# Kernel tuning notes

Measured on AMD Instinct MI355X. Metric: run time of the kernel, lower is better.

Reference implementation:

```python
import jax, jax.numpy as jnp
import numpy as np

B, T = 4, 2048          # batch, seq_len
D, H = 2048, 4096       # input_dim, router hidden_dim
E, O = 16, 2048         # num_experts, expert_output_dim
TAU = 0.5               # forward default tau


def setup_inputs() -> dict:
    key = jax.random.key(0)
    kx, k1, k2, k3, k4, k5, k6 = jax.random.split(key, 7)
    s = 0.02
    return {
        "x": jax.random.normal(kx, (B, T, D), dtype=jnp.float32),
        "W1": jax.random.normal(k1, (D, H), dtype=jnp.float32) * s,
        "b1": jnp.zeros((H,), dtype=jnp.float32),
        "W2": jax.random.normal(k2, (H, E), dtype=jnp.float32) * s,
        "b2": jnp.zeros((E,), dtype=jnp.float32),
        "We": jax.random.normal(k3, (E, D, O), dtype=jnp.float32) * s,
        "be": jnp.zeros((E, O), dtype=jnp.float32),
    }


def reference(x, W1, b1, W2, b2, We, be):
    # Router: Linear -> ReLU -> Linear -> softmax
    h = jax.nn.relu(jnp.einsum("btd,dh->bth", x, W1) + b1)
    logits = jnp.einsum("bth,he->bte", h, W2) + b2
    probs = jax.nn.softmax(logits, axis=-1)                 # [B,T,E]
    max_p = jnp.max(probs, axis=-1, keepdims=True)
    mask = probs >= TAU * max_p                              # [B,T,E] bool
    k_per_token = jnp.sum(mask, axis=-1)                     # [B,T] int
    gates = jnp.where(mask, probs, 0.0)                      # masked router probs
    # Per-expert dense Linear, masked weighted accumulate (E=16 is a fixed,
    # structurally distinct set; loop is over experts, not data dims).
    out = jnp.zeros((B, T, O), dtype=x.dtype)
    for i in range(E):
        expert_out = jnp.einsum("btd,do->bto", x, We[i]) + be[i]
        out = out + gates[..., i:i + 1] * expert_out
    return out, k_per_token
```

## Files before the change

### kernel.cpp

```cpp
#include <hip/hip_runtime.h>
#include <stdint.h>

#define M_TOK 8192
#define DDIM  2048
#define HDIM  4096
#define NEXP  16
#define ODIM  2048

typedef __attribute__((ext_vector_type(8))) __bf16 bf16x8;
typedef __attribute__((ext_vector_type(4))) float  f32x4;

__device__ __forceinline__ unsigned short f2bf(float f) {
    unsigned int u = __float_as_uint(f);
    unsigned int r = (u + 0x7FFFu + ((u >> 16) & 1u)) >> 16;
    return (unsigned short)r;
}
__device__ __forceinline__ float bf2f(unsigned short s) {
    return __uint_as_float(((unsigned int)s) << 16);
}


__global__ void split_x_kernel(const float* __restrict__ x,
                               ushort* __restrict__ xh, ushort* __restrict__ xl) {
    size_t i = ((size_t)blockIdx.x * 256 + threadIdx.x) * 4;
    float4 v = *(const float4*)(x + i);
    float f[4] = {v.x, v.y, v.z, v.w};
    ushort hu[4], lu[4];
#pragma unroll
    for (int u = 0; u < 4; ++u) {
        hu[u] = f2bf(f[u]);
        lu[u] = f2bf(f[u] - bf2f(hu[u]));
    }
    *(ushort4*)(xh + i) = make_ushort4(hu[0], hu[1], hu[2], hu[3]);
    *(ushort4*)(xl + i) = make_ushort4(lu[0], lu[1], lu[2], lu[3]);
}

__global__ void transpose_split_w1_kernel(const float* __restrict__ W1,
                                          ushort* __restrict__ th, ushort* __restrict__ tl) {
    __shared__ float tile[64][65];
    int h0 = (blockIdx.x & 63) * 64;
    int d0 = (blockIdx.x >> 6) * 64;
    int r = threadIdx.x >> 4;
    int c = (threadIdx.x & 15) * 4;
#pragma unroll
    for (int rr = 0; rr < 4; ++rr) {
        int row = rr * 16 + r;
        float4 v = *(const float4*)(W1 + (size_t)(d0 + row) * HDIM + h0 + c);
        tile[row][c + 0] = v.x; tile[row][c + 1] = v.y;
        tile[row][c + 2] = v.z; tile[row][c + 3] = v.w;
    }
    __syncthreads();
#pragma unroll
    for (int rr = 0; rr < 4; ++rr) {
        int hrow = rr * 16 + r;
        ushort hu[4], lu[4];
#pragma unroll
        for (int u = 0; u < 4; ++u) {
            float f = tile[c + u][hrow];
            hu[u] = f2bf(f);
            lu[u] = f2bf(f - bf2f(hu[u]));
        }
        size_t o = (size_t)(h0 + hrow) * DDIM + d0 + c;
        *(ushort4*)(th + o) = make_ushort4(hu[0], hu[1], hu[2], hu[3]);
        *(ushort4*)(tl + o) = make_ushort4(lu[0], lu[1], lu[2], lu[3]);
    }
}

__global__ void transpose_we_kernel(const float* __restrict__ We, ushort* __restrict__ wt) {
    __shared__ float tile[64][65];
    int e = blockIdx.y;
    int o0 = (blockIdx.x & 31) * 64;
    int d0 = (blockIdx.x >> 5) * 64;
    const float* src = We + (size_t)e * DDIM * ODIM;
    ushort* dst = wt + (size_t)e * ODIM * DDIM;
    int r = threadIdx.x >> 4;
    int c = (threadIdx.x & 15) * 4;
#pragma unroll
    for (int rr = 0; rr < 4; ++rr) {
        int row = rr * 16 + r;
        float4 v = *(const float4*)(src + (size_t)(d0 + row) * ODIM + o0 + c);
        tile[row][c + 0] = v.x; tile[row][c + 1] = v.y;
        tile[row][c + 2] = v.z; tile[row][c + 3] = v.w;
    }
    __syncthreads();
#pragma unroll
    for (int rr = 0; rr < 4; ++rr) {
        int orow = rr * 16 + r;
        ushort hu[4];
#pragma unroll
        for (int u = 0; u < 4; ++u) hu[u] = f2bf(tile[c + u][orow]);
        *(ushort4*)(dst + (size_t)(o0 + orow) * DDIM + d0 + c) =
            make_ushort4(hu[0], hu[1], hu[2], hu[3]);
    }
}


__device__ __forceinline__ void stage_tile(const ushort* __restrict__ g0, int ld,
                                           ushort* lds0, int wave, int lane) {
#pragma unroll
    for (int j = 0; j < 4; ++j) {
        int L = wave * 256 + j * 64 + lane;
        int m = L >> 3;
        int kc = (L & 7) ^ (m & 7);
        const ushort* gp = g0 + (size_t)m * ld + kc * 8;
        ushort* lp = lds0 + (size_t)(wave * 256 + j * 64) * 8;
        __builtin_amdgcn_global_load_lds(
            (const __attribute__((address_space(1))) void*)gp,
            (__attribute__((address_space(3))) void*)lp, 16, 0, 0);
    }
}

__device__ __forceinline__ bf16x8 ldfrag(const ushort* lds0, int row, int kc) {
    return *(const bf16x8*)(lds0 + ((row << 3) + (kc ^ (row & 7))) * 8);
}

__global__ __launch_bounds__(256, 2) void gemm1_kernel(
    const ushort* __restrict__ xh, const ushort* __restrict__ xl,
    const ushort* __restrict__ wh, const ushort* __restrict__ wl,
    const float* __restrict__ b1, float* __restrict__ hout) {
    __shared__ ushort As[8192];
    __shared__ ushort Bs[8192];
    const int tile_m = (blockIdx.x & 63) << 7;
    const int tile_n = (blockIdx.x >> 6) << 7;
    const int tid = threadIdx.x;
    const int wave = tid >> 6, lane = tid & 63;
    const int q = lane >> 4, mrow = lane & 15;
    const int wm = (wave >> 1) << 6, wn = (wave & 1) << 6;
    f32x4 acc[4][4];
#pragma unroll
    for (int i = 0; i < 4; ++i)
#pragma unroll
        for (int j = 0; j < 4; ++j) acc[i][j] = {0.f, 0.f, 0.f, 0.f};

    for (int it = 0; it < 96; ++it) {
        const int phase = it >> 5;
        const ushort* Ab = (phase == 1) ? xl : xh;
        const ushort* Bb = (phase == 2) ? wl : wh;
        const int k0 = (it & 31) << 6;
        __syncthreads();
        stage_tile(Ab + (size_t)tile_m * DDIM + k0, DDIM, As, wave, lane);
        stage_tile(Bb + (size_t)tile_n * DDIM + k0, DDIM, Bs, wave, lane);
        __syncthreads();
#pragma unroll
        for (int s = 0; s < 2; ++s) {
            bf16x8 af[4], bfr[4];
#pragma unroll
            for (int i = 0; i < 4; ++i) af[i] = ldfrag(As, wm + i * 16 + mrow, s * 4 + q);
#pragma unroll
            for (int j = 0; j < 4; ++j) bfr[j] = ldfrag(Bs, wn + j * 16 + mrow, s * 4 + q);
#pragma unroll
            for (int i = 0; i < 4; ++i)
#pragma unroll
                for (int j = 0; j < 4; ++j)
                    acc[i][j] = __builtin_amdgcn_mfma_f32_16x16x32_bf16(
                        af[i], bfr[j], acc[i][j], 0, 0, 0);
        }
    }
#pragma unroll
    for (int i = 0; i < 4; ++i) {
        const int r0 = tile_m + wm + i * 16 + q * 4;
#pragma unroll
        for (int j = 0; j < 4; ++j) {
            const int cc = tile_n + wn + j * 16 + mrow;
            const float bb = b1[cc];
#pragma unroll
            for (int r = 0; r < 4; ++r) {
                float v = acc[i][j][r] + bb;
                hout[(size_t)(r0 + r) * HDIM + cc] = v > 0.f ? v : 0.f;
            }
        }
    }
}

__global__ void gemm2_kernel(const float* __restrict__ h, const float* __restrict__ W2,
                             const float* __restrict__ b2, float* __restrict__ logits) {
    const int e = threadIdx.x & 15;
    const int t = blockIdx.x * 16 + (threadIdx.x >> 4);
    const float* hr = h + (size_t)t * HDIM;
    float acc = 0.f;
    for (int d = 0; d < HDIM; d += 8) {
#pragma unroll
        for (int u = 0; u < 8; ++u)
            acc = fmaf(hr[d + u], W2[(size_t)(d + u) * NEXP + e], acc);
    }
    logits[(size_t)t * NEXP + e] = acc + b2[e];
}

__global__ void gates_kernel(const float* __restrict__ logits,
                             float* __restrict__ gates, float* __restrict__ kout,
                             int* __restrict__ cnt, int* __restrict__ list) {
    const int t = blockIdx.x * 256 + threadIdx.x;
    float l[16];
    const float4* lp = (const float4*)(logits + (size_t)t * 16);
#pragma unroll
    for (int i = 0; i < 4; ++i) {
        float4 v = lp[i];
        l[i * 4] = v.x; l[i * 4 + 1] = v.y; l[i * 4 + 2] = v.z; l[i * 4 + 3] = v.w;
    }
    float lmax = l[0];
#pragma unroll
    for (int i = 1; i < 16; ++i) lmax = fmaxf(lmax, l[i]);
    float p[16], S = 0.f;
#pragma unroll
    for (int i = 0; i < 16; ++i) { p[i] = expf(l[i] - lmax); S += p[i]; }
#pragma unroll
    for (int i = 0; i < 16; ++i) p[i] /= S;
    float pmax = p[0];
#pragma unroll
    for (int i = 1; i < 16; ++i) pmax = fmaxf(pmax, p[i]);
    const float thr = 0.5f * pmax;
    int k = 0;
    float g[16];
#pragma unroll
    for (int i = 0; i < 16; ++i) {
        bool m = p[i] >= thr;
        g[i] = m ? p[i] : 0.f;
        k += m ? 1 : 0;
        if (m) {
            int pos = atomicAdd(&cnt[i], 1);
            list[i * M_TOK + pos] = t;
        }
    }
    float4* gp = (float4*)(gates + (size_t)t * 16);
#pragma unroll
    for (int i = 0; i < 4; ++i)
        gp[i] = make_float4(g[i * 4], g[i * 4 + 1], g[i * 4 + 2], g[i * 4 + 3]);
    kout[t] = (float)k;
}

__global__ void init_out_kernel(const float* __restrict__ gates,
                                const float* __restrict__ be, float* __restrict__ out) {
    const int t = blockIdx.x;
    const int tid = threadIdx.x;
    __shared__ float g[16];
    if (tid < 16) g[tid] = gates[(size_t)t * 16 + tid];
    __syncthreads();
    const int c0 = tid * 8;
    float a[8] = {0.f, 0.f, 0.f, 0.f, 0.f, 0.f, 0.f, 0.f};
#pragma unroll
    for (int e = 0; e < 16; ++e) {
        float ge = g[e];
        if (ge != 0.f) {
            float4 v1 = *(const float4*)(be + (size_t)e * ODIM + c0);
            float4 v2 = *(const float4*)(be + (size_t)e * ODIM + c0 + 4);
            a[0] = fmaf(ge, v1.x, a[0]); a[1] = fmaf(ge, v1.y, a[1]);
            a[2] = fmaf(ge, v1.z, a[2]); a[3] = fmaf(ge, v1.w, a[3]);
            a[4] = fmaf(ge, v2.x, a[4]); a[5] = fmaf(ge, v2.y, a[5]);
            a[6] = fmaf(ge, v2.z, a[6]); a[7] = fmaf(ge, v2.w, a[7]);
        }
    }
    *(float4*)(out + (size_t)t * ODIM + c0)     = make_float4(a[0], a[1], a[2], a[3]);
    *(float4*)(out + (size_t)t * ODIM + c0 + 4) = make_float4(a[4], a[5], a[6], a[7]);
}

__global__ __launch_bounds__(256, 3) void moe_sparse_kernel(
    const ushort* __restrict__ xh, const ushort* __restrict__ weT,
    const float* __restrict__ gates, const int* __restrict__ cnt,
    const int* __restrict__ list, float* __restrict__ out) {
    const int bx = blockIdx.x;
    const int e = bx >> 10;
    const int chunk = (bx >> 4) & 63;
    const int ntile = bx & 15;
    const int ce = cnt[e];
    const int row0 = chunk << 7;
    if (row0 >= ce) return;
    const int rows = min(128, ce - row0);

    __shared__ ushort As[8192];
    __shared__ ushort Bs[8192];
    __shared__ int toks[128];
    __shared__ float gv[128];

    const int tid = threadIdx.x;
    if (tid < 128) {
        int t = list[e * M_TOK + row0 + min(tid, rows - 1)];
        toks[tid] = t;
        gv[tid] = gates[(size_t)t * NEXP + e];
    }
    __syncthreads();

    const int wave = tid >> 6, lane = tid & 63;
    const int q = lane >> 4, mrow = lane & 15;
    const int wm = (wave >> 1) << 6, wn = (wave & 1) << 6;

    const ushort* agp[4];
    const ushort* bgp[4];
    ushort* alp[4];
    ushort* blp[4];
    const ushort* wbase = weT + ((size_t)e * ODIM + (ntile << 7)) * DDIM;
#pragma unroll
    for (int j = 0; j < 4; ++j) {
        int L = wave * 256 + j * 64 + lane;
        int m = L >> 3;
        int kc = (L & 7) ^ (m & 7);
        agp[j] = xh + (size_t)toks[m] * DDIM + kc * 8;
        bgp[j] = wbase + (size_t)m * DDIM + kc * 8;
        alp[j] = As + (size_t)L * 8;
        blp[j] = Bs + (size_t)L * 8;
    }

    f32x4 acc[4][4];
#pragma unroll
    for (int i = 0; i < 4; ++i)
#pragma unroll
        for (int j = 0; j < 4; ++j) acc[i][j] = {0.f, 0.f, 0.f, 0.f};

    for (int it = 0; it < 32; ++it) {
        const int k0 = it << 6;
        __syncthreads();
#pragma unroll
        for (int j = 0; j < 4; ++j) {
            __builtin_amdgcn_global_load_lds(
                (const __attribute__((address_space(1))) void*)(agp[j] + k0),
                (__attribute__((address_space(3))) void*)alp[j], 16, 0, 0);
            __builtin_amdgcn_global_load_lds(
                (const __attribute__((address_space(1))) void*)(bgp[j] + k0),
                (__attribute__((address_space(3))) void*)blp[j], 16, 0, 0);
        }
        __syncthreads();
#pragma unroll
        for (int s = 0; s < 2; ++s) {
            bf16x8 af[4], bfr[4];
#pragma unroll
            for (int i = 0; i < 4; ++i) af[i] = ldfrag(As, wm + i * 16 + mrow, s * 4 + q);
#pragma unroll
            for (int j = 0; j < 4; ++j) bfr[j] = ldfrag(Bs, wn + j * 16 + mrow, s * 4 + q);
#pragma unroll
            for (int i = 0; i < 4; ++i)
#pragma unroll
                for (int j = 0; j < 4; ++j)
                    acc[i][j] = __builtin_amdgcn_mfma_f32_16x16x32_bf16(
                        af[i], bfr[j], acc[i][j], 0, 0, 0);
        }
    }

#pragma unroll
    for (int i = 0; i < 4; ++i) {
        const int rl = wm + i * 16 + q * 4;
#pragma unroll
        for (int r = 0; r < 4; ++r) {
            const int lrow = rl + r;
            if (lrow < rows) {
                const int t = toks[lrow];
                const float g = gv[lrow];
                float* orow = out + (size_t)t * ODIM + (ntile << 7) + wn + mrow;
#pragma unroll
                for (int j = 0; j < 4; ++j)
                    atomicAdd(orow + j * 16, g * acc[i][j][r]);
            }
        }
    }
}

extern "C" void kernel_launch(void* const* d_in, const int* in_sizes, int n_in,
                              void* d_out, int out_size, void* d_ws, size_t ws_size,
                              hipStream_t stream) {
    const float* x  = (const float*)d_in[0];
    const float* W1 = (const float*)d_in[1];
    const float* b1 = (const float*)d_in[2];
    const float* W2 = (const float*)d_in[3];
    const float* b2 = (const float*)d_in[4];
    const float* We = (const float*)d_in[5];
    const float* be = (const float*)d_in[6];
    float* out  = (float*)d_out;
    float* kout = out + (size_t)M_TOK * ODIM;

    char* ws = (char*)d_ws;
    ushort* x_hi   = (ushort*)(ws);
    ushort* x_lo   = (ushort*)(ws + 33554432);
    ushort* w1t_hi = (ushort*)(ws + 67108864);
    ushort* w1t_lo = (ushort*)(ws + 83886080);
    int*    cnt    = (int*)   (ws + 83886080);
    int*    list   = (int*)   (ws + 83887104);
    float*  hbuf   = (float*) (ws + 100663296);
    ushort* weT    = (ushort*)(ws + 100663296);
    float*  logits = (float*) (ws + 234881024);
    float*  gates  = (float*) (ws + 235405312);

    split_x_kernel<<<16384, 256, 0, stream>>>(x, x_hi, x_lo);
    transpose_split_w1_kernel<<<2048, 256, 0, stream>>>(W1, w1t_hi, w1t_lo);
    gemm1_kernel<<<2048, 256, 0, stream>>>(x_hi, x_lo, w1t_hi, w1t_lo, b1, hbuf);
    gemm2_kernel<<<512, 256, 0, stream>>>(hbuf, W2, b2, logits);
    hipMemsetAsync(cnt, 0, 64, stream);
    gates_kernel<<<32, 256, 0, stream>>>(logits, gates, kout, cnt, list);
    dim3 gwe(1024, 16);
    transpose_we_kernel<<<gwe, 256, 0, stream>>>(We, weT);
    init_out_kernel<<<M_TOK, 256, 0, stream>>>(gates, be, out);
    moe_sparse_kernel<<<16384, 256, 0, stream>>>(x_hi, weT, gates, cnt, list, out);
}
```

Before: 1.334 ms.

## Fuse router second linear into gemm1 epilogue with atomic logit accumulation

The ReLU hidden activations are no longer written to a 128 MB global buffer and re-read by a separate gemm2 kernel. Instead each gemm1 tile multiplies its ReLU outputs by the matching W2 rows in registers, reduces across lanes with DPP adds, combines the two column-waves through LDS, and atomically adds partial logits into a zeroed buffer. The b2 bias moves into the gates kernel. This trades a large memory round trip for a heavier epilogue with extra registers and 32 atomic contributions per logit, and the floating-point summation order becomes nondeterministic.

```diff
diff --git a/kernel.cpp b/kernel.cpp
--- a/kernel.cpp
+++ b/kernel.cpp
@@ -17,6 +17,12 @@
 }
 __device__ __forceinline__ float bf2f(unsigned short s) {
     return __uint_as_float(((unsigned int)s) << 16);
+}
+
+template <int CTRL>
+__device__ __forceinline__ float dpp_add(float x) {
+    int yi = __builtin_amdgcn_update_dpp(0, __float_as_int(x), CTRL, 0xF, 0xF, true);
+    return x + __int_as_float(yi);
 }
 
 
@@ -117,7 +123,8 @@
 __global__ __launch_bounds__(256, 2) void gemm1_kernel(
     const ushort* __restrict__ xh, const ushort* __restrict__ xl,
     const ushort* __restrict__ wh, const ushort* __restrict__ wl,
-    const float* __restrict__ b1, float* __restrict__ hout) {
+    const float* __restrict__ b1, const float* __restrict__ W2,
+    float* __restrict__ logits) {
     __shared__ ushort As[8192];
     __shared__ ushort Bs[8192];
     const int tile_m = (blockIdx.x & 63) << 7;
@@ -156,37 +163,66 @@
                         af[i], bfr[j], acc[i][j], 0, 0, 0);
         }
     }
+
+    float b1v[4];
+    f32x4 w2r[4][4];
+#pragma unroll
+    for (int j = 0; j < 4; ++j) {
+        const int cc = tile_n + wn + j * 16 + mrow;
+        b1v[j] = b1[cc];
+        const float4* wp = (const float4*)(W2 + (size_t)cc * NEXP);
+#pragma unroll
+        for (int qq = 0; qq < 4; ++qq) {
+            float4 v = wp[qq];
+            w2r[j][qq] = (f32x4){v.x, v.y, v.z, v.w};
+        }
+    }
+    __syncthreads();
+    float* part = (float*)As;
+    const int w01 = wave & 1;
 #pragma unroll
     for (int i = 0; i < 4; ++i) {
-        const int r0 = tile_m + wm + i * 16 + q * 4;
-#pragma unroll
-        for (int j = 0; j < 4; ++j) {
-            const int cc = tile_n + wn + j * 16 + mrow;
-            const float bb = b1[cc];
-#pragma unroll
-            for (int r = 0; r < 4; ++r) {
-                float v = acc[i][j][r] + bb;
-                hout[(size_t)(r0 + r) * HDIM + cc] = v > 0.f ? v : 0.f;
+#pragma unroll
+        for (int r = 0; r < 4; ++r) {
+            const int rl = wm + i * 16 + q * 4 + r;
+            float ll[16];
+#pragma unroll
+            for (int e = 0; e < 16; ++e) ll[e] = 0.f;
+#pragma unroll
+            for (int j = 0; j < 4; ++j) {
+                float v = acc[i][j][r] + b1v[j];
+                v = v > 0.f ? v : 0.f;
+#pragma unroll
+                for (int e = 0; e < 16; ++e)
+                    ll[e] = fmaf(v, w2r[j][e >> 2][e & 3], ll[e]);
             }
-        }
-    }
-}
-
-__global__ void gemm2_kernel(const float* __restrict__ h, const float* __restrict__ W2,
-                             const float* __restrict__ b2, float* __restrict__ logits) {
-    const int e = threadIdx.x & 15;
-    const int t = blockIdx.x * 16 + (threadIdx.x >> 4);
-    const float* hr = h + (size_t)t * HDIM;
-    float acc = 0.f;
-    for (int d = 0; d < HDIM; d += 8) {
-#pragma unroll
-        for (int u = 0; u < 8; ++u)
-            acc = fmaf(hr[d + u], W2[(size_t)(d + u) * NEXP + e], acc);
-    }
-    logits[(size_t)t * NEXP + e] = acc + b2[e];
+#pragma unroll
+            for (int e = 0; e < 16; ++e) {
+                float v = ll[e];
+                v = dpp_add<0xB1>(v);
+                v = dpp_add<0x4E>(v);
+                v = dpp_add<0x124>(v);
+                v = dpp_add<0x128>(v);
+                ll[e] = v;
+            }
+            if (mrow == 0) {
+                float4* dst = (float4*)(part + ((size_t)(w01 * 128 + rl)) * 16);
+                dst[0] = make_float4(ll[0],  ll[1],  ll[2],  ll[3]);
+                dst[1] = make_float4(ll[4],  ll[5],  ll[6],  ll[7]);
+                dst[2] = make_float4(ll[8],  ll[9],  ll[10], ll[11]);
+                dst[3] = make_float4(ll[12], ll[13], ll[14], ll[15]);
+            }
+        }
+    }
+    __syncthreads();
+    for (int idx = tid; idx < 2048; idx += 256) {
+        float s = part[idx] + part[2048 + idx];
+        atomicAdd(&logits[(size_t)(tile_m + (idx >> 4)) * NEXP + (idx & 15)], s);
+    }
 }
 
 __global__ void gates_kernel(const float* __restrict__ logits,
+                             const float* __restrict__ b2,
                              float* __restrict__ gates, float* __restrict__ kout,
                              int* __restrict__ cnt, int* __restrict__ list) {
     const int t = blockIdx.x * 256 + threadIdx.x;
@@ -197,6 +233,8 @@
         float4 v = lp[i];
         l[i * 4] = v.x; l[i * 4 + 1] = v.y; l[i * 4 + 2] = v.z; l[i * 4 + 3] = v.w;
     }
+#pragma unroll
+    for (int i = 0; i < 16; ++i) l[i] += b2[i];
     float lmax = l[0];
 #pragma unroll
     for (int i = 1; i < 16; ++i) lmax = fmaxf(lmax, l[i]);
@@ -372,17 +410,16 @@
     ushort* w1t_lo = (ushort*)(ws + 83886080);
     int*    cnt    = (int*)   (ws + 83886080);
     int*    list   = (int*)   (ws + 83887104);
-    float*  hbuf   = (float*) (ws + 100663296);
     ushort* weT    = (ushort*)(ws + 100663296);
     float*  logits = (float*) (ws + 234881024);
     float*  gates  = (float*) (ws + 235405312);
 
+    hipMemsetAsync(logits, 0, (size_t)M_TOK * NEXP * sizeof(float), stream);
     split_x_kernel<<<16384, 256, 0, stream>>>(x, x_hi, x_lo);
     transpose_split_w1_kernel<<<2048, 256, 0, stream>>>(W1, w1t_hi, w1t_lo);
-    gemm1_kernel<<<2048, 256, 0, stream>>>(x_hi, x_lo, w1t_hi, w1t_lo, b1, hbuf);
-    gemm2_kernel<<<512, 256, 0, stream>>>(hbuf, W2, b2, logits);
+    gemm1_kernel<<<2048, 256, 0, stream>>>(x_hi, x_lo, w1t_hi, w1t_lo, b1, W2, logits);
     hipMemsetAsync(cnt, 0, 64, stream);
-    gates_kernel<<<32, 256, 0, stream>>>(logits, gates, kout, cnt, list);
+    gates_kernel<<<32, 256, 0, stream>>>(logits, b2, gates, kout, cnt, list);
     dim3 gwe(1024, 16);
     transpose_we_kernel<<<gwe, 256, 0, stream>>>(We, weT);
     init_out_kernel<<<M_TOK, 256, 0, stream>>>(gates, be, out);
```

Result: faster. 1.208 ms (-9.5%).
